# Performance work log

Measured on AMD Instinct MI355X. Metric: run time of the kernel, lower is better.

## Reference

```python
import jax, jax.numpy as jnp
import numpy as np

NC, NT = 3072, 1024   # context / target counts
D, H, L, FF = 256, 8, 2, 1024  # token_dim, heads, icl_layers, ffn hidden
HD = D // H


def _ln(x, g, b, eps=1e-5):
    m = x.mean(-1, keepdims=True)
    v = ((x - m) ** 2).mean(-1, keepdims=True)
    return (x - m) / jnp.sqrt(v + eps) * g + b


def setup_inputs() -> dict:
    key = jax.random.key(0)
    ks = jax.random.split(key, 16)
    s = 0.02  # weight init scale
    return {
        "c_ctx": jax.random.normal(ks[0], (NC, D), jnp.float32),
        "c_tgt": jax.random.normal(ks[1], (NT, D), jnp.float32),
        "y_context": jax.random.uniform(ks[2], (NC,), jnp.float32),
        "exposure_context": jax.random.uniform(ks[3], (NC,), jnp.float32),
        "exposure_target": jax.random.uniform(ks[4], (NT,), jnp.float32),
        "dec_W1": jax.random.normal(ks[5], (1, D), jnp.float32) * s,
        "dec_b1": jnp.zeros((D,), jnp.float32),
        "dec_W2": jax.random.normal(ks[6], (D, D), jnp.float32) * s,
        "dec_b2": jnp.zeros((D,), jnp.float32),
        "log_kappa": jnp.zeros((1,), jnp.float32),
        "WQ": jax.random.normal(ks[7], (L, D, D), jnp.float32) * s,
        "bQ": jnp.zeros((L, D), jnp.float32),
        "WK": jax.random.normal(ks[8], (L, D, D), jnp.float32) * s,
        "bK": jnp.zeros((L, D), jnp.float32),
        "WV": jax.random.normal(ks[9], (L, D, D), jnp.float32) * s,
        "bV": jnp.zeros((L, D), jnp.float32),
        "WO": jax.random.normal(ks[10], (L, D, D), jnp.float32) * s,
        "bO": jnp.zeros((L, D), jnp.float32),
        "ln1_g": jnp.ones((L, D), jnp.float32),
        "ln1_b": jnp.zeros((L, D), jnp.float32),
        "ln2_g": jnp.ones((L, D), jnp.float32),
        "ln2_b": jnp.zeros((L, D), jnp.float32),
        "ffn_W1": jax.random.normal(ks[11], (L, D, FF), jnp.float32) * s,
        "ffn_b1": jnp.zeros((L, FF), jnp.float32),
        "ffn_W2": jax.random.normal(ks[12], (L, FF, D), jnp.float32) * s,
        "ffn_b2": jnp.zeros((L, D), jnp.float32),
        "out_W": jax.random.normal(ks[13], (D, 1), jnp.float32) * s,
        "out_b": jnp.zeros((1,), jnp.float32),
    }


def reference(c_ctx, c_tgt, y_context, exposure_context, exposure_target,
              dec_W1, dec_b1, dec_W2, dec_b2, log_kappa,
              WQ, bQ, WK, bK, WV, bV, WO, bO,
              ln1_g, ln1_b, ln2_g, ln2_b,
              ffn_W1, ffn_b1, ffn_W2, ffn_b2, out_W, out_b):
    n = NC + NT
    # --- OutcomeTokenDecorator (eq 2.4) ---
    kappa = jax.nn.softplus(log_kappa[0])
    exp_all = jnp.concatenate([exposure_context, exposure_target])        # (n,)
    y_all = jnp.concatenate([y_context, jnp.zeros((NT,), y_context.dtype)])
    c_all = jnp.concatenate([c_ctx, c_tgt], axis=0)                       # (n, D)
    w = exp_all / (exp_all + kappa)                                       # (n,)
    y_emb = jnp.tanh(y_all[:, None] @ dec_W1 + dec_b1) @ dec_W2 + dec_b2  # (n, D)
    ctx_mask = jnp.concatenate([jnp.ones((NC,), jnp.float32), jnp.zeros((NT,), jnp.float32)])
    c = c_all + (w * ctx_mask)[:, None] * y_emb

    # --- target-target blocking additive mask M^inf ---
    is_target = jnp.concatenate([jnp.zeros((NC,), bool), jnp.ones((NT,), bool)])
    both_target = is_target[:, None] & is_target[None, :]
    mask_add = jnp.where(both_target & ~jnp.eye(n, dtype=bool), -jnp.inf, 0.0)  # (n, n)

    scale = jnp.sqrt(jnp.float32(HD))
    for l in range(L):  # fixed small number of structurally distinct layers
        Q = (c @ WQ[l] + bQ[l]).reshape(n, H, HD)
        K = (c @ WK[l] + bK[l]).reshape(n, H, HD)
        V = (c @ WV[l] + bV[l]).reshape(n, H, HD)
        scores = jnp.einsum('qhd,khd->hqk', Q, K) / scale + mask_add      # (H, n, n)
        attn = jax.nn.softmax(scores, axis=-1)
        o = jnp.einsum('hqk,khd->qhd', attn, V).reshape(n, D)
        o = o @ WO[l] + bO[l]
        c = _ln(c + o, ln1_g[l], ln1_b[l])
        f = jax.nn.relu(c @ ffn_W1[l] + ffn_b1[l]) @ ffn_W2[l] + ffn_b2[l]
        c = _ln(c + f, ln2_g[l], ln2_b[l])

    log_mu = (c[NC:] @ out_W + out_b)[:, 0]                               # (NT,)
    return jnp.exp(log_mu) * exposure_target
```

## Files before the change

### kernel.cpp

```cpp
#include <hip/hip_runtime.h>
#include <hip/hip_bf16.h>
#include <math.h>

#define NC_   3072
#define NT_   1024
#define NTOK  4096
#define DD    256
#define NH    8
#define HDIM  32
#define NL    2
#define FFD   1024

typedef __attribute__((ext_vector_type(8))) short short8;
typedef __attribute__((ext_vector_type(4))) float f32x4;

#if __has_builtin(__builtin_amdgcn_exp2f)
#define EXP2(x) __builtin_amdgcn_exp2f(x)
#else
#define EXP2(x) exp2f(x)
#endif

#define QSCALE 0.25503482964f

__device__ inline float bf2f(ushort u) { return __uint_as_float(((unsigned)u) << 16); }
__device__ inline ushort f2bf(float x) {
    __hip_bfloat16 h = __float2bfloat16(x);
    return *reinterpret_cast<ushort*>(&h);
}
__device__ inline void gload16(const void* g, void* l) {
    __builtin_amdgcn_global_load_lds(
        (const __attribute__((address_space(1))) void*)g,
        (__attribute__((address_space(3))) void*)l, 16, 0, 0);
}

__global__ __launch_bounds__(256) void convert_kernel(
    const float* __restrict__ WQ, const float* __restrict__ WK,
    const float* __restrict__ WV, const float* __restrict__ WO,
    const float* __restrict__ W1, const float* __restrict__ W2,
    const float* __restrict__ bQ, const float* __restrict__ bK,
    const float* __restrict__ bV, const float* __restrict__ dW2,
    const float* __restrict__ y_context, const float* __restrict__ dec_W1,
    const float* __restrict__ dec_b1, ushort* __restrict__ tv,
    ushort* __restrict__ wbf, float* __restrict__ bqkv)
{
    int l = blockIdx.y;
    int idx = blockIdx.x * 256 + threadIdx.x;
    if (idx >= 852736) {
        if (l != 0) return;
        int i2 = idx - 852736;
        int m = i2 >> 6, k = (i2 & 63) * 4;
        float y = (m < NC_) ? y_context[m] : 0.f;
        ushort4 u;
        u.x = f2bf(tanhf(y * dec_W1[k+0] + dec_b1[k+0]));
        u.y = f2bf(tanhf(y * dec_W1[k+1] + dec_b1[k+1]));
        u.z = f2bf(tanhf(y * dec_W1[k+2] + dec_b1[k+2]));
        u.w = f2bf(tanhf(y * dec_W1[k+3] + dec_b1[k+3]));
        *(ushort4*)&tv[(size_t)i2 * 4] = u;
        return;
    }
    if (idx >= 787200) {
        if (l != 0) return;
        int i = idx - 787200;
        int n = i >> 8, k = i & 255;
        wbf[(size_t)2*786432 + i] = f2bf(dW2[(size_t)k*256 + n]);
        return;
    }
    if (idx >= 786432) {
        int i = idx - 786432;
        float bv = (i < 256) ? bQ[l*256 + i]
                 : (i < 512) ? bK[l*256 + (i - 256)]
                             : bV[l*256 + (i - 512)];
        bqkv[l*768 + i] = bv;
        return;
    }
    float v;
    if (idx < 196608) {
        int n = idx >> 8, k = idx & 255;
        v = (n < 256) ? WQ[(size_t)(l*256 + k)*256 + n]
          : (n < 512) ? WK[(size_t)(l*256 + k)*256 + (n-256)]
                      : WV[(size_t)(l*256 + k)*256 + (n-512)];
    } else if (idx < 262144) {
        int i = idx - 196608, n = i >> 8, k = i & 255;
        v = WO[(size_t)(l*256 + k)*256 + n];
    } else if (idx < 524288) {
        int i = idx - 262144, n = i >> 8, k = i & 255;
        v = W1[(size_t)(l*256 + k)*1024 + n];
    } else {
        int i = idx - 524288, n = i >> 10, k = i & 1023;
        v = W2[(size_t)(l*1024 + k)*256 + n];
    }
    wbf[(size_t)l*786432 + idx] = f2bf(v);
}

__global__ __launch_bounds__(256) void gemm_bf(
    const ushort* __restrict__ A, const ushort* __restrict__ Bt,
    const float* __restrict__ bias, void* __restrict__ Cv, void* __restrict__ Cv2,
    int M, int N, int K, int mode,
    const float* __restrict__ xc, const float* __restrict__ ca,
    const float* __restrict__ cb, const float* __restrict__ lk)
{
    __shared__ ushort As[64*64];
    __shared__ ushort Bs[64*64];
    int tid = threadIdx.x, lane = tid & 63, w = tid >> 6;
    int wm = w >> 1, wn = w & 1;
    int m0 = blockIdx.y * 64, n0 = blockIdx.x * 64;
    int col = lane & 15, grp = lane >> 4;
    f32x4 acc[2][2] = {};

    for (int k0 = 0; k0 < K; k0 += 64) {
        __syncthreads();
        #pragma unroll
        for (int s = 0; s < 2; ++s) {
            int i = tid + s*256;
            int r = i >> 3, j = i & 7;
            int kb = (j*16) ^ ((r & 7) << 4);
            gload16((const char*)(A  + (size_t)(m0 + r)*K + k0) + kb,
                    (char*)As + s*4096 + w*1024);
            gload16((const char*)(Bt + (size_t)(n0 + r)*K + k0) + kb,
                    (char*)Bs + s*4096 + w*1024);
        }
        __syncthreads();
        #pragma unroll
        for (int kk = 0; kk < 64; kk += 32) {
            short8 a[2], b[2];
            #pragma unroll
            for (int f = 0; f < 2; ++f) {
                int ra = wm*32 + f*16 + col;
                a[f] = *(const short8*)((char*)As + ra*128 + (((kk + grp*8)*2) ^ ((ra & 7) << 4)));
                int rb = wn*32 + f*16 + col;
                b[f] = *(const short8*)((char*)Bs + rb*128 + (((kk + grp*8)*2) ^ ((rb & 7) << 4)));
            }
            #pragma unroll
            for (int fm = 0; fm < 2; ++fm)
                #pragma unroll
                for (int fn = 0; fn < 2; ++fn)
                    acc[fm][fn] = __builtin_amdgcn_mfma_f32_16x16x32_bf16(a[fm], b[fn], acc[fm][fn], 0, 0, 0);
        }
    }
    float kap = (mode == 5) ? log1pf(expf(lk[0])) : 0.f;
    #pragma unroll
    for (int fm = 0; fm < 2; ++fm) {
        #pragma unroll
        for (int fn = 0; fn < 2; ++fn) {
            int ncol = n0 + wn*32 + fn*16 + col;
            int mbase = m0 + wm*32 + fm*16 + grp*4;
            float bs = bias[ncol];
            if (mode == 4 && ncol >= 512) {
                ushort* base = (ushort*)Cv2 - (size_t)512*M;
                ushort4 u;
                u.x = f2bf(acc[fm][fn][0] + bs); u.y = f2bf(acc[fm][fn][1] + bs);
                u.z = f2bf(acc[fm][fn][2] + bs); u.w = f2bf(acc[fm][fn][3] + bs);
                *(ushort4*)(base + (size_t)ncol*M + mbase) = u;
            } else if (mode == 4) {
                int cc = ncol & 255, hh = cc >> 5, hd = cc & 31;
                ushort* base = (ushort*)Cv + ((ncol < 256) ? 0u : 1048576u);
                float sc = (ncol < 256) ? QSCALE : 1.f;
                #pragma unroll
                for (int r = 0; r < 4; ++r)
                    base[((size_t)hh*M + mbase + r)*HDIM + hd] = f2bf((acc[fm][fn][r] + bs) * sc);
            } else if (mode == 5) {
                #pragma unroll
                for (int r = 0; r < 4; ++r) {
                    int m = mbase + r;
                    float basev = (m < NC_) ? ca[(size_t)m*DD + ncol]
                                            : cb[(size_t)(m - NC_)*DD + ncol];
                    float wv = 0.f;
                    if (m < NC_) { float e = xc[m]; wv = e / (e + kap); }
                    float v = basev + wv * (acc[fm][fn][r] + bs);
                    ((float*)Cv)[(size_t)m*DD + ncol] = v;
                    ((ushort*)Cv2)[(size_t)m*DD + ncol] = f2bf(v);
                }
            } else {
                #pragma unroll
                for (int r = 0; r < 4; ++r) {
                    float v = acc[fm][fn][r] + bs;
                    if (mode == 3) v = fmaxf(v, 0.f);
                    if (mode == 0) ((float*)Cv)[(size_t)(mbase + r)*N + ncol] = v;
                    else           ((ushort*)Cv)[(size_t)(mbase + r)*N + ncol] = f2bf(v);
                }
            }
        }
    }
}

__global__ __launch_bounds__(1024, 8) void attn_kernel(
    const ushort* __restrict__ Qh, const ushort* __restrict__ Kh,
    const ushort* __restrict__ Vt, ushort* __restrict__ AO,
    float* __restrict__ pml, float* __restrict__ pacc, int l2mode)
{
    __shared__ __align__(16) char smem[37888];
    __shared__ float cml[16][16];
    int tid = threadIdx.x;
    int w = tid >> 6, lane = tid & 63;
    int q = lane & 15, g = lane >> 4;
    int wq = w & 3, kh = w >> 2;
    int h = blockIdx.y;
    int zb = blockIdx.z;
    int q0   = l2mode ? (NC_ + blockIdx.x * 64) : (blockIdx.x * 64);
    int kbeg = l2mode ? zb * 1536 : 0;
    int do_self = l2mode ? (zb == 0) : (q0 >= NC_);
    int nt = l2mode ? 12 : (((q0 >= NC_) ? NC_ : NTOK) >> 7);

    short8 bq = *(const short8*)&Qh[((size_t)h*NTOK + q0 + wq*16 + q)*HDIM + g*8];
    short8 ones;
    #pragma unroll
    for (int e = 0; e < 8; ++e) ones[e] = (short)0x3F80;

    f32x4 acc0 = {0.f,0.f,0.f,0.f}, acc1 = {0.f,0.f,0.f,0.f};
    f32x4 accl = {0.f,0.f,0.f,0.f};
    const f32x4 z = {0.f,0.f,0.f,0.f};

    const ushort* src0;
    char *dst0, *dst1;
    size_t sstep;
    if (w < 8) {
        int L  = (w << 3) + (lane >> 3);
        int s  = lane & 7;
        int e  = s ^ (L & 7);
        int r  = 2*L + (e >> 2);
        int qt = e & 3;
        int ch = r >> 5, rr = r & 31;
        int hi = (rr >> 4) & 1, qp = rr & 15;
        int key = ch*32 + (((qp >> 2) << 3) | (hi << 2) | (qp & 3));
        src0 = Kh + ((size_t)h*NTOK + kbeg + key)*HDIM + qt*8;
        sstep = (size_t)128*HDIM;
        dst0 = smem + w*1024;
        dst1 = dst0 + 8192;
    } else {
        int u = w - 8;
        int d = u*4 + (lane >> 4);
        int s = lane & 15;
        int e = (s & 8) | ((s ^ (d & 7)) & 7);
        src0 = Vt + ((size_t)(h*HDIM + d))*NTOK + kbeg + e*8;
        sstep = 128;
        dst0 = smem + 16384 + u*1024;
        dst1 = dst0 + 8192;
    }
    gload16(src0, dst0);
    asm volatile("s_waitcnt vmcnt(0)" ::: "memory");
    __builtin_amdgcn_s_barrier();
    __builtin_amdgcn_sched_barrier(0);

    const int L0 = kh*16 + (q >> 1);
    const char* kb0 = smem + L0*128 + (((((q & 1) << 2) + g) ^ (L0 & 7)) << 4);
    const int vslot = (kh << 2) + g;
    const int vsx = (vslot & 8) | ((vslot ^ (q & 7)) & 7);
    const char* vb0 = smem + 16384 + q*256 + (vsx << 4);
    const char* vb1 = vb0 + 16*256;

#define ATTN_TILE(BUF, TT)                                                               \
    {                                                                                    \
        if ((TT) + 1 < nt)                                                               \
            gload16(src0 + (size_t)((TT)+1)*sstep, (BUF) ? dst0 : dst1);                 \
        short8 ka0 = *(const short8*)(kb0 + (BUF)*8192);                                 \
        short8 ka1 = *(const short8*)(kb0 + (BUF)*8192 + 1024);                          \
        __builtin_amdgcn_s_setprio(1);                                                   \
        f32x4 st0 = __builtin_amdgcn_mfma_f32_16x16x32_bf16(ka0, bq, z, 0, 0, 0);        \
        f32x4 st1 = __builtin_amdgcn_mfma_f32_16x16x32_bf16(ka1, bq, z, 0, 0, 0);        \
        __builtin_amdgcn_s_setprio(0);                                                   \
        float p0 = EXP2(st0[0]), p1 = EXP2(st0[1]);                                      \
        float p2 = EXP2(st0[2]), p3 = EXP2(st0[3]);                                      \
        float p4 = EXP2(st1[0]), p5 = EXP2(st1[1]);                                      \
        float p6 = EXP2(st1[2]), p7 = EXP2(st1[3]);                                      \
        uint4 pw;                                                                        \
        pw.x = (__float_as_uint(p0) >> 16) | (__float_as_uint(p1) & 0xFFFF0000u);        \
        pw.y = (__float_as_uint(p2) >> 16) | (__float_as_uint(p3) & 0xFFFF0000u);        \
        pw.z = (__float_as_uint(p4) >> 16) | (__float_as_uint(p5) & 0xFFFF0000u);        \
        pw.w = (__float_as_uint(p6) >> 16) | (__float_as_uint(p7) & 0xFFFF0000u);        \
        short8 pf = *(short8*)&pw;                                                       \
        short8 va0 = *(const short8*)(vb0 + (BUF)*8192);                                 \
        short8 va1 = *(const short8*)(vb1 + (BUF)*8192);                                 \
        __builtin_amdgcn_s_setprio(1);                                                   \
        acc0 = __builtin_amdgcn_mfma_f32_16x16x32_bf16(va0, pf, acc0, 0, 0, 0);          \
        acc1 = __builtin_amdgcn_mfma_f32_16x16x32_bf16(va1, pf, acc1, 0, 0, 0);          \
        accl = __builtin_amdgcn_mfma_f32_16x16x32_bf16(ones, pf, accl, 0, 0, 0);         \
        __builtin_amdgcn_s_setprio(0);                                                   \
        if ((TT) + 1 < nt) {                                                             \
            asm volatile("s_waitcnt vmcnt(0)" ::: "memory");                             \
            __builtin_amdgcn_s_barrier();                                                \
            __builtin_amdgcn_sched_barrier(0);                                           \
        }                                                                                \
    }

    for (int t = 0; t < nt; t += 2) {
        ATTN_TILE(0, t)
        ATTN_TILE(1, t + 1)
    }
#undef ATTN_TILE

    float lsum = accl[0];

    if (do_self && kh == 0) {
        int qg = q0 + wq*16 + q;
        short8 kv = *(const short8*)&Kh[((size_t)h*NTOK + qg)*HDIM + g*8];
        float d8 = 0.f;
        #pragma unroll
        for (int e = 0; e < 8; ++e) d8 += bf2f((ushort)bq[e]) * bf2f((ushort)kv[e]);
        d8 += __shfl_xor(d8, 16, 64);
        d8 += __shfl_xor(d8, 32, 64);
        float pp = EXP2(d8);
        lsum += pp;
        #pragma unroll
        for (int r = 0; r < 4; ++r) {
            acc0[r] += pp * bf2f(Vt[(size_t)(h*HDIM + g*4 + r)*NTOK + qg]);
            acc1[r] += pp * bf2f(Vt[(size_t)(h*HDIM + 16 + g*4 + r)*NTOK + qg]);
        }
    }

    __syncthreads();
    float* cacc = (float*)smem;
    #pragma unroll
    for (int r = 0; r < 4; ++r) {
        cacc[(w*32 + g*4 + r)*17 + q]      = acc0[r];
        cacc[(w*32 + 16 + g*4 + r)*17 + q] = acc1[r];
    }
    if (g == 0) cml[w][q] = lsum;
    __syncthreads();

    if (w < 4) {
        float L = cml[w][q] + cml[w+4][q] + cml[w+8][q] + cml[w+12][q];
        if (!l2mode) {
            float inv = 1.f / L;
            ushort* dst = AO + (size_t)(q0 + w*16 + q)*DD + h*HDIM;
            ushort4 o0, o1;
            #pragma unroll
            for (int r = 0; r < 4; ++r) {
                int e0 = g*4 + r, e1 = 16 + g*4 + r;
                float O0 = cacc[(w*32+e0)*17+q] + cacc[((w+4)*32+e0)*17+q]
                         + cacc[((w+8)*32+e0)*17+q] + cacc[((w+12)*32+e0)*17+q];
                float O1 = cacc[(w*32+e1)*17+q] + cacc[((w+4)*32+e1)*17+q]
                         + cacc[((w+8)*32+e1)*17+q] + cacc[((w+12)*32+e1)*17+q];
                ((ushort*)&o0)[r] = f2bf(O0 * inv);
                ((ushort*)&o1)[r] = f2bf(O1 * inv);
            }
            *(ushort4*)(dst + g*4) = o0;
            *(ushort4*)(dst + 16 + g*4) = o1;
        } else {
            int qi = q0 - NC_ + w*16 + q;
            float* pa = pacc + (((size_t)zb*NH + h)*NT_ + qi)*32;
            #pragma unroll
            for (int r = 0; r < 4; ++r) {
                int e0 = g*4 + r, e1 = 16 + g*4 + r;
                pa[e0] = cacc[(w*32+e0)*17+q] + cacc[((w+4)*32+e0)*17+q]
                       + cacc[((w+8)*32+e0)*17+q] + cacc[((w+12)*32+e0)*17+q];
                pa[e1] = cacc[(w*32+e1)*17+q] + cacc[((w+4)*32+e1)*17+q]
                       + cacc[((w+8)*32+e1)*17+q] + cacc[((w+12)*32+e1)*17+q];
            }
            if (g == 0) pml[((size_t)zb*NH + h)*NT_ + qi] = L;
        }
    }
}

__global__ __launch_bounds__(256) void combine_kernel(
    const float* __restrict__ pml, const float* __restrict__ pacc, ushort* __restrict__ AO)
{
    int item = blockIdx.x * 8 + (threadIdx.x >> 5);
    int d = threadIdx.x & 31;
    int hh = item >> 10, qi = item & 1023;
    size_t i0 = ((size_t)0*NH + hh)*NT_ + qi;
    size_t i1 = ((size_t)1*NH + hh)*NT_ + qi;
    float inv = 1.f / (pml[i0] + pml[i1]);
    float O = pacc[i0*32 + d] + pacc[i1*32 + d];
    AO[(size_t)(NC_ + qi)*DD + hh*HDIM + d] = f2bf(O * inv);
}

__global__ __launch_bounds__(256) void ln_kernel(
    float* __restrict__ c, const float* __restrict__ delta,
    const float* __restrict__ g, const float* __restrict__ b, ushort* __restrict__ cbf,
    const float* __restrict__ ow, const float* __restrict__ ob,
    const float* __restrict__ expo, float* __restrict__ out)
{
    int tid = threadIdx.x;
    int wid = tid >> 6, lane = tid & 63;
    int row = blockIdx.x * 4 + wid;
    float4 x  = *(const float4*)&c[(size_t)row*DD + lane*4];
    float4 dl = *(const float4*)&delta[(size_t)row*DD + lane*4];
    x.x += dl.x; x.y += dl.y; x.z += dl.z; x.w += dl.w;
    float s = x.x + x.y + x.z + x.w;
    #pragma unroll
    for (int off = 1; off < 64; off <<= 1) s += __shfl_xor(s, off, 64);
    float mean = s * (1.f/DD);
    float dx = x.x-mean, dy = x.y-mean, dz = x.z-mean, dw = x.w-mean;
    float v = dx*dx + dy*dy + dz*dz + dw*dw;
    #pragma unroll
    for (int off = 1; off < 64; off <<= 1) v += __shfl_xor(v, off, 64);
    float rstd = rsqrtf(v*(1.f/DD) + 1e-5f);
    float4 g4 = *(const float4*)&g[lane*4];
    float4 b4 = *(const float4*)&b[lane*4];
    float4 o;
    o.x = dx*rstd*g4.x + b4.x;
    o.y = dy*rstd*g4.y + b4.y;
    o.z = dz*rstd*g4.z + b4.z;
    o.w = dw*rstd*g4.w + b4.w;
    *(float4*)&c[(size_t)row*DD + lane*4] = o;
    ushort4 u;
    u.x = f2bf(o.x); u.y = f2bf(o.y); u.z = f2bf(o.z); u.w = f2bf(o.w);
    *(ushort4*)&cbf[(size_t)row*DD + lane*4] = u;
    if (ow != nullptr) {
        float4 wv = *(const float4*)&ow[lane*4];
        float ss = o.x*wv.x + o.y*wv.y + o.z*wv.z + o.w*wv.w;
        #pragma unroll
        for (int off = 1; off < 64; off <<= 1) ss += __shfl_xor(ss, off, 64);
        if (lane == 0) out[row] = expf(ss + ob[0]) * expo[row];
    }
}

extern "C" void kernel_launch(void* const* d_in, const int* in_sizes, int n_in,
                              void* d_out, int out_size, void* d_ws, size_t ws_size,
                              hipStream_t stream) {
    const float* c_ctx            = (const float*)d_in[0];
    const float* c_tgt            = (const float*)d_in[1];
    const float* y_context        = (const float*)d_in[2];
    const float* exposure_context = (const float*)d_in[3];
    const float* exposure_target  = (const float*)d_in[4];
    const float* dec_W1           = (const float*)d_in[5];
    const float* dec_b1           = (const float*)d_in[6];
    const float* dec_W2           = (const float*)d_in[7];
    const float* dec_b2           = (const float*)d_in[8];
    const float* log_kappa        = (const float*)d_in[9];
    const float* WQ               = (const float*)d_in[10];
    const float* bQ               = (const float*)d_in[11];
    const float* WK               = (const float*)d_in[12];
    const float* bK               = (const float*)d_in[13];
    const float* WV               = (const float*)d_in[14];
    const float* bV               = (const float*)d_in[15];
    const float* WO               = (const float*)d_in[16];
    const float* bO               = (const float*)d_in[17];
    const float* ln1_g            = (const float*)d_in[18];
    const float* ln1_b            = (const float*)d_in[19];
    const float* ln2_g            = (const float*)d_in[20];
    const float* ln2_b            = (const float*)d_in[21];
    const float* ffn_W1           = (const float*)d_in[22];
    const float* ffn_b1           = (const float*)d_in[23];
    const float* ffn_W2           = (const float*)d_in[24];
    const float* ffn_b2           = (const float*)d_in[25];
    const float* out_W            = (const float*)d_in[26];
    const float* out_b            = (const float*)d_in[27];
    float* out = (float*)d_out;

    float* ws = (float*)d_ws;
    float*  c    = ws;
    float*  T    = ws + 1048576;
    ushort* ub   = (ushort*)(ws + 2097152);
    ushort* c_bf = ub;
    ushort* Qh   = ub + 1048576;
    ushort* Khb  = ub + 2097152;
    ushort* Vt   = ub + 3145728;
    ushort* AO   = ub + 4194304;
    ushort* wbf  = ub + 5242880;
    ushort* wdec = wbf + 1572864;
    float*  bqkv = (float*)(ub + 6881280);
    ushort* tv   = AO;
    ushort* Hd   = Qh;
    float*  pml  = T;
    float*  pacc = T + 16384;

    convert_kernel<<<dim3(4355, 2), 256, 0, stream>>>(WQ, WK, WV, WO, ffn_W1, ffn_W2,
                                                      bQ, bK, bV, dec_W2,
                                                      y_context, dec_W1, dec_b1, tv,
                                                      wbf, bqkv);
    gemm_bf<<<dim3(4, 64), 256, 0, stream>>>(tv, wdec, dec_b2, c, c_bf, NTOK, DD, DD, 5,
                                             exposure_context, c_ctx, c_tgt, log_kappa);
    {
        ushort* wl = wbf;
        gemm_bf<<<dim3(12, 64), 256, 0, stream>>>(c_bf, wl, bqkv, Qh, Vt, NTOK, 768, DD, 4,
                                                  nullptr, nullptr, nullptr, nullptr);
        attn_kernel<<<dim3(64, NH, 1), 1024, 0, stream>>>(Qh, Khb, Vt, AO, nullptr, nullptr, 0);
        gemm_bf<<<dim3(4, 64),  256, 0, stream>>>(AO, wl + 196608, bO, T, nullptr, NTOK, DD, DD, 0,
                                                  nullptr, nullptr, nullptr, nullptr);
        ln_kernel<<<NTOK/4, 256, 0, stream>>>(c, T, ln1_g, ln1_b, c_bf,
                                              nullptr, nullptr, nullptr, nullptr);
        gemm_bf<<<dim3(16, 64), 256, 0, stream>>>(c_bf, wl + 262144, ffn_b1, Hd, nullptr, NTOK, FFD, DD, 3,
                                                  nullptr, nullptr, nullptr, nullptr);
        gemm_bf<<<dim3(4, 64),  256, 0, stream>>>(Hd, wl + 524288, ffn_b2, T, nullptr, NTOK, DD, FFD, 0,
                                                  nullptr, nullptr, nullptr, nullptr);
        ln_kernel<<<NTOK/4, 256, 0, stream>>>(c, T, ln2_g, ln2_b, c_bf,
                                              nullptr, nullptr, nullptr, nullptr);
    }
    {
        ushort* wl = wbf + 786432;
        gemm_bf<<<dim3(12, 64), 256, 0, stream>>>(c_bf, wl, bqkv + 768, Qh, Vt, NTOK, 768, DD, 4,
                                                  nullptr, nullptr, nullptr, nullptr);
        attn_kernel<<<dim3(16, NH, 2), 1024, 0, stream>>>(Qh, Khb, Vt, AO, pml, pacc, 1);
        combine_kernel<<<1024, 256, 0, stream>>>(pml, pacc, AO);
        gemm_bf<<<dim3(4, 16),  256, 0, stream>>>(AO + (size_t)NC_*DD, wl + 196608, bO + DD, T, nullptr,
                                                  NT_, DD, DD, 0, nullptr, nullptr, nullptr, nullptr);
        ln_kernel<<<NT_/4, 256, 0, stream>>>(c + (size_t)NC_*DD, T, ln1_g + DD, ln1_b + DD,
                                             c_bf + (size_t)NC_*DD,
                                             nullptr, nullptr, nullptr, nullptr);
        gemm_bf<<<dim3(16, 16), 256, 0, stream>>>(c_bf + (size_t)NC_*DD, wl + 262144, ffn_b1 + FFD,
                                                  Hd, nullptr, NT_, FFD, DD, 3,
                                                  nullptr, nullptr, nullptr, nullptr);
        gemm_bf<<<dim3(4, 16),  256, 0, stream>>>(Hd, wl + 524288, ffn_b2 + DD, T, nullptr,
                                                  NT_, DD, FFD, 0, nullptr, nullptr, nullptr, nullptr);
        ln_kernel<<<NT_/4, 256, 0, stream>>>(c + (size_t)NC_*DD, T, ln2_g + DD, ln2_b + DD,
                                             c_bf + (size_t)NC_*DD,
                                             out_W, out_b, exposure_target, out);
    }
}
```

Baseline: 142.4 us.

## Deepen attention K/V prefetch to four buffers and skip unused layer-2 Q tiles

The attention kernel moves from double to quad buffering in shared memory. It keeps two tile loads in flight with vmcnt(1) waits and unrolls the loop by four, so load latency is better hidden. Shared memory grows to 64KB per block, which may cut occupancy. Separately, the layer-2 QKV GEMM now skips the Q-column blocks for context rows, since only target queries are used in the last layer.

```diff
diff --git a/kernel.cpp b/kernel.cpp
--- a/kernel.cpp
+++ b/kernel.cpp
@@ -95,10 +95,11 @@
 __global__ __launch_bounds__(256) void gemm_bf(
     const ushort* __restrict__ A, const ushort* __restrict__ Bt,
     const float* __restrict__ bias, void* __restrict__ Cv, void* __restrict__ Cv2,
-    int M, int N, int K, int mode,
+    int M, int N, int K, int mode, int qskip,
     const float* __restrict__ xc, const float* __restrict__ ca,
     const float* __restrict__ cb, const float* __restrict__ lk)
 {
+    if (mode == 4 && qskip && blockIdx.x < 4 && blockIdx.y < 48) return;
     __shared__ ushort As[64*64];
     __shared__ ushort Bs[64*64];
     int tid = threadIdx.x, lane = tid & 63, w = tid >> 6;
@@ -188,7 +189,7 @@
     const ushort* __restrict__ Vt, ushort* __restrict__ AO,
     float* __restrict__ pml, float* __restrict__ pacc, int l2mode)
 {
-    __shared__ __align__(16) char smem[37888];
+    __shared__ __align__(16) char smem[65536];
     __shared__ float cml[16][16];
     int tid = threadIdx.x;
     int w = tid >> 6, lane = tid & 63;
@@ -211,7 +212,7 @@
     const f32x4 z = {0.f,0.f,0.f,0.f};
 
     const ushort* src0;
-    char *dst0, *dst1;
+    char* dst0;
     size_t sstep;
     if (w < 8) {
         int L  = (w << 3) + (lane >> 3);
@@ -225,7 +226,6 @@
         src0 = Kh + ((size_t)h*NTOK + kbeg + key)*HDIM + qt*8;
         sstep = (size_t)128*HDIM;
         dst0 = smem + w*1024;
-        dst1 = dst0 + 8192;
     } else {
         int u = w - 8;
         int d = u*4 + (lane >> 4);
@@ -233,11 +233,11 @@
         int e = (s & 8) | ((s ^ (d & 7)) & 7);
         src0 = Vt + ((size_t)(h*HDIM + d))*NTOK + kbeg + e*8;
         sstep = 128;
-        dst0 = smem + 16384 + u*1024;
-        dst1 = dst0 + 8192;
+        dst0 = smem + 32768 + u*1024;
     }
     gload16(src0, dst0);
-    asm volatile("s_waitcnt vmcnt(0)" ::: "memory");
+    gload16(src0 + sstep, dst0 + 8192);
+    asm volatile("s_waitcnt vmcnt(1)" ::: "memory");
     __builtin_amdgcn_s_barrier();
     __builtin_amdgcn_sched_barrier(0);
 
@@ -245,13 +245,13 @@
     const char* kb0 = smem + L0*128 + (((((q & 1) << 2) + g) ^ (L0 & 7)) << 4);
     const int vslot = (kh << 2) + g;
     const int vsx = (vslot & 8) | ((vslot ^ (q & 7)) & 7);
-    const char* vb0 = smem + 16384 + q*256 + (vsx << 4);
+    const char* vb0 = smem + 32768 + q*256 + (vsx << 4);
     const char* vb1 = vb0 + 16*256;
 
 #define ATTN_TILE(BUF, TT)                                                               \
     {                                                                                    \
-        if ((TT) + 1 < nt)                                                               \
-            gload16(src0 + (size_t)((TT)+1)*sstep, (BUF) ? dst0 : dst1);                 \
+        if ((TT) + 2 < nt)                                                               \
+            gload16(src0 + (size_t)((TT)+2)*sstep, dst0 + (((BUF)+2)&3)*8192);           \
         short8 ka0 = *(const short8*)(kb0 + (BUF)*8192);                                 \
         short8 ka1 = *(const short8*)(kb0 + (BUF)*8192 + 1024);                          \
         __builtin_amdgcn_s_setprio(1);                                                   \
@@ -276,15 +276,20 @@
         accl = __builtin_amdgcn_mfma_f32_16x16x32_bf16(ones, pf, accl, 0, 0, 0);         \
         __builtin_amdgcn_s_setprio(0);                                                   \
         if ((TT) + 1 < nt) {                                                             \
-            asm volatile("s_waitcnt vmcnt(0)" ::: "memory");                             \
+            if ((TT) + 2 < nt)                                                           \
+                asm volatile("s_waitcnt vmcnt(1)" ::: "memory");                         \
+            else                                                                         \
+                asm volatile("s_waitcnt vmcnt(0)" ::: "memory");                         \
             __builtin_amdgcn_s_barrier();                                                \
             __builtin_amdgcn_sched_barrier(0);                                           \
         }                                                                                \
     }
 
-    for (int t = 0; t < nt; t += 2) {
+    for (int t = 0; t < nt; t += 4) {
         ATTN_TILE(0, t)
         ATTN_TILE(1, t + 1)
+        ATTN_TILE(2, t + 2)
+        ATTN_TILE(3, t + 3)
     }
 #undef ATTN_TILE
 
@@ -459,40 +464,40 @@
                                                       bQ, bK, bV, dec_W2,
                                                       y_context, dec_W1, dec_b1, tv,
                                                       wbf, bqkv);
-    gemm_bf<<<dim3(4, 64), 256, 0, stream>>>(tv, wdec, dec_b2, c, c_bf, NTOK, DD, DD, 5,
+    gemm_bf<<<dim3(4, 64), 256, 0, stream>>>(tv, wdec, dec_b2, c, c_bf, NTOK, DD, DD, 5, 0,
                                              exposure_context, c_ctx, c_tgt, log_kappa);
     {
         ushort* wl = wbf;
-        gemm_bf<<<dim3(12, 64), 256, 0, stream>>>(c_bf, wl, bqkv, Qh, Vt, NTOK, 768, DD, 4,
+        gemm_bf<<<dim3(12, 64), 256, 0, stream>>>(c_bf, wl, bqkv, Qh, Vt, NTOK, 768, DD, 4, 0,
                                                   nullptr, nullptr, nullptr, nullptr);
         attn_kernel<<<dim3(64, NH, 1), 1024, 0, stream>>>(Qh, Khb, Vt, AO, nullptr, nullptr, 0);
-        gemm_bf<<<dim3(4, 64),  256, 0, stream>>>(AO, wl + 196608, bO, T, nullptr, NTOK, DD, DD, 0,
+        gemm_bf<<<dim3(4, 64),  256, 0, stream>>>(AO, wl + 196608, bO, T, nullptr, NTOK, DD, DD, 0, 0,
                                                   nullptr, nullptr, nullptr, nullptr);
         ln_kernel<<<NTOK/4, 256, 0, stream>>>(c, T, ln1_g, ln1_b, c_bf,
                                               nullptr, nullptr, nullptr, nullptr);
-        gemm_bf<<<dim3(16, 64), 256, 0, stream>>>(c_bf, wl + 262144, ffn_b1, Hd, nullptr, NTOK, FFD, DD, 3,
+        gemm_bf<<<dim3(16, 64), 256, 0, stream>>>(c_bf, wl + 262144, ffn_b1, Hd, nullptr, NTOK, FFD, DD, 3, 0,
                                                   nullptr, nullptr, nullptr, nullptr);
-        gemm_bf<<<dim3(4, 64),  256, 0, stream>>>(Hd, wl + 524288, ffn_b2, T, nullptr, NTOK, DD, FFD, 0,
+        gemm_bf<<<dim3(4, 64),  256, 0, stream>>>(Hd, wl + 524288, ffn_b2, T, nullptr, NTOK, DD, FFD, 0, 0,
                                                   nullptr, nullptr, nullptr, nullptr);
         ln_kernel<<<NTOK/4, 256, 0, stream>>>(c, T, ln2_g, ln2_b, c_bf,
                                               nullptr, nullptr, nullptr, nullptr);
     }
     {
         ushort* wl = wbf + 786432;
-        gemm_bf<<<dim3(12, 64), 256, 0, stream>>>(c_bf, wl, bqkv + 768, Qh, Vt, NTOK, 768, DD, 4,
+        gemm_bf<<<dim3(12, 64), 256, 0, stream>>>(c_bf, wl, bqkv + 768, Qh, Vt, NTOK, 768, DD, 4, 1,
                                                   nullptr, nullptr, nullptr, nullptr);
         attn_kernel<<<dim3(16, NH, 2), 1024, 0, stream>>>(Qh, Khb, Vt, AO, pml, pacc, 1);
         combine_kernel<<<1024, 256, 0, stream>>>(pml, pacc, AO);
         gemm_bf<<<dim3(4, 16),  256, 0, stream>>>(AO + (size_t)NC_*DD, wl + 196608, bO + DD, T, nullptr,
-                                                  NT_, DD, DD, 0, nullptr, nullptr, nullptr, nullptr);
+                                                  NT_, DD, DD, 0, 0, nullptr, nullptr, nullptr, nullptr);
         ln_kernel<<<NT_/4, 256, 0, stream>>>(c + (size_t)NC_*DD, T, ln1_g + DD, ln1_b + DD,
                                              c_bf + (size_t)NC_*DD,
                                              nullptr, nullptr, nullptr, nullptr);
         gemm_bf<<<dim3(16, 16), 256, 0, stream>>>(c_bf + (size_t)NC_*DD, wl + 262144, ffn_b1 + FFD,
-                                                  Hd, nullptr, NT_, FFD, DD, 3,
+                                                  Hd, nullptr, NT_, FFD, DD, 3, 0,
                                                   nullptr, nullptr, nullptr, nullptr);
         gemm_bf<<<dim3(4, 16),  256, 0, stream>>>(Hd, wl + 524288, ffn_b2 + DD, T, nullptr,
-                                                  NT_, DD, FFD, 0, nullptr, nullptr, nullptr, nullptr);
+                                                  NT_, DD, FFD, 0, 0, nullptr, nullptr, nullptr, nullptr);
         ln_kernel<<<NT_/4, 256, 0, stream>>>(c + (size_t)NC_*DD, T, ln2_g + DD, ln2_b + DD,
                                              c_bf + (size_t)NC_*DD,
                                              out_W, out_b, exposure_target, out);
```

New measurement: 142.8 us. Within noise of the previous version (+0.3%).
